# Optimization experiments

Measured on AMD Instinct MI355X. Metric: run time of the kernel, lower is better.

Reference implementation:

```python
import jax, jax.numpy as jnp
import numpy as np

T_MAX = 20
NUM_HEADS = 8
COMPLEXITY_W = 0.3
LN_EPS = 1e-5


def _layernorm(h, g, b):
    mu = jnp.mean(h, axis=-1, keepdims=True)
    var = jnp.var(h, axis=-1, keepdims=True)
    return (h - mu) / jnp.sqrt(var + LN_EPS) * g + b


def _gate_mlp(x, W1, b1, g, be, W2, b2, W3, b3):
    # Linear -> LayerNorm -> ReLU -> (Dropout=id in eval) -> Linear -> ReLU -> Linear -> Sigmoid
    h = jax.nn.relu(_layernorm(x @ W1 + b1, g, be))
    h = jax.nn.relu(h @ W2 + b2)
    return jax.nn.sigmoid(h @ W3 + b3)


def _adaptive_windows(x, p):
    S = x.shape[1]
    gate = _gate_mlp(x, p['gW1'], p['gb1'], p['gg'], p['gbe'], p['gW2'], p['gb2'], p['gW3'], p['gb3'])
    comp = _gate_mlp(x, p['cW1'], p['cb1'], p['cg'], p['cbe'], p['cW2'], p['cb2'], p['cW3'], p['cb3'])
    pos = jnp.linspace(0.8, 1.2, S, dtype=x.dtype).reshape(1, -1, 1)
    score = ((1.0 - COMPLEXITY_W) * gate + COMPLEXITY_W * comp) * pos
    T_i = jnp.clip(jnp.ceil(score[..., 0] * T_MAX), 1, T_MAX).astype(jnp.int32)  # [B,S]
    return T_i


def _spike_sum(x, T_i, alpha, beta):
    # LIF recurrence over T_MAX steps; accumulate masked spikes. x: [B,S,E]
    z = jnp.zeros_like(x)

    def step(carry, t):
        v, i, acc = carry
        active = (t < T_i).astype(x.dtype)[..., None]  # [B,S,1]
        i = alpha * i + x * active
        v = beta * v + i
        s = (v >= 1.0).astype(x.dtype)
        v = v * (1.0 - s)  # v_reset = 0
        return (v, i, acc + s * active), None

    (_, _, acc), _ = jax.lax.scan(step, (z, z, z), jnp.arange(T_MAX))
    return acc


def _forward(x, params):
    B, S, E = x.shape
    H, D = NUM_HEADS, E // NUM_HEADS
    q = x @ params['Wq']
    k = x @ params['Wk']
    v = x @ params['Wv']
    T_i = _adaptive_windows(x, params)
    q_sum = _spike_sum(q, T_i, params['alpha_q'], params['beta_q'])
    k_sum = _spike_sum(k, T_i, params['alpha_k'], params['beta_k'])
    v_mean = _spike_sum(v, T_i, params['alpha_v'], params['beta_v']) / T_MAX
    q_sum = q_sum.reshape(B, S, H, D)
    k_sum = k_sum.reshape(B, S, H, D)
    v_mean = v_mean.reshape(B, S, H, D)
    scale = D ** -0.5
    scores = jnp.einsum('bihd,bjhd->bhij', q_sum, k_sum) * scale
    w = jax.nn.softmax(scores, axis=-1)
    out = jnp.einsum('bhij,bjhd->bihd', w, v_mean).reshape(B, S, E)
    return out @ params['Wo'] + params['bo']


def setup_inputs() -> dict:
    key = jax.random.key(0)
    ks = iter(jax.random.split(key, 32))
    B, S, E = 4, 1024, 512
    f32 = jnp.float32

    def w(shape, scale=0.02):
        return jax.random.normal(next(ks), shape, dtype=f32) * scale

    inp = {
        'x': jax.random.normal(next(ks), (B, S, E), dtype=f32),
        'Wq': w((E, E)), 'Wk': w((E, E)), 'Wv': w((E, E)),
        'Wo': w((E, E)), 'bo': jnp.zeros((E,), f32),
        'gW1': w((E, 128)), 'gb1': jnp.zeros((128,), f32),
        'gg': jnp.ones((128,), f32), 'gbe': jnp.zeros((128,), f32),
        'gW2': w((128, 64)), 'gb2': jnp.zeros((64,), f32),
        'gW3': w((64, 1)), 'gb3': jnp.zeros((1,), f32),
        'cW1': w((E, 64)), 'cb1': jnp.zeros((64,), f32),
        'cg': jnp.ones((64,), f32), 'cbe': jnp.zeros((64,), f32),
        'cW2': w((64, 32)), 'cb2': jnp.zeros((32,), f32),
        'cW3': w((32, 1)), 'cb3': jnp.zeros((1,), f32),
        'alpha_q': jnp.asarray(np.exp(-1 / 5.0), f32), 'beta_q': jnp.asarray(np.exp(-1 / 20.0), f32),
        'alpha_k': jnp.asarray(np.exp(-1 / 5.0), f32), 'beta_k': jnp.asarray(np.exp(-1 / 20.0), f32),
        'alpha_v': jnp.asarray(np.exp(-1 / 5.0), f32), 'beta_v': jnp.asarray(np.exp(-1 / 20.0), f32),
    }
    return inp


def reference(x, Wq, Wk, Wv, Wo, bo,
              gW1, gb1, gg, gbe, gW2, gb2, gW3, gb3,
              cW1, cb1, cg, cbe, cW2, cb2, cW3, cb3,
              alpha_q, beta_q, alpha_k, beta_k, alpha_v, beta_v):
    params = dict(Wq=Wq, Wk=Wk, Wv=Wv, Wo=Wo, bo=bo,
                  gW1=gW1, gb1=gb1, gg=gg, gbe=gbe, gW2=gW2, gb2=gb2, gW3=gW3, gb3=gb3,
                  cW1=cW1, cb1=cb1, cg=cg, cbe=cbe, cW2=cW2, cb2=cb2, cW3=cW3, cb3=cb3,
                  alpha_q=alpha_q, beta_q=beta_q, alpha_k=alpha_k, beta_k=beta_k,
                  alpha_v=alpha_v, beta_v=beta_v)
    return _forward(x, params)
```

## Files before the change

### kernel.cpp

```cpp
#include <hip/hip_runtime.h>
#include <math.h>

#define SEQ   1024
#define EMB   512
#define NROWS 4096
#define LDP   72
#define GROWS 4

typedef __attribute__((ext_vector_type(8))) short short8;
typedef __attribute__((ext_vector_type(4))) float float4v;

__device__ __forceinline__ float bf2f(unsigned short s) {
    union { float f; unsigned u; } x; x.u = ((unsigned)s) << 16; return x.f;
}
__device__ __forceinline__ unsigned short f2bf(float f) {
    union { float f; unsigned u; } x; x.f = f;
    unsigned r = x.u + 0x7fffu + ((x.u >> 16) & 1u);
    return (unsigned short)(r >> 16);
}

__device__ __forceinline__ void gld16(const unsigned short* g, short* l) {
    __builtin_amdgcn_global_load_lds(
        (__attribute__((address_space(1))) void*)(g),
        (__attribute__((address_space(3))) void*)(l), 16, 0, 0);
}

__device__ __forceinline__ void split3(float x, unsigned short& h, unsigned short& m, unsigned short& l) {
    union { float f; unsigned u; } a; a.f = x;
    const unsigned rh = a.u + 0x7fffu + ((a.u >> 16) & 1u);
    h = (unsigned short)(rh >> 16);
    union { float f; unsigned u; } hf; hf.u = rh & 0xffff0000u;
    const float r1 = x - hf.f;
    a.f = r1;
    const unsigned rm = a.u + 0x7fffu + ((a.u >> 16) & 1u);
    m = (unsigned short)(rm >> 16);
    union { float f; unsigned u; } mf; mf.u = rm & 0xffff0000u;
    const float r2 = r1 - mf.f;
    l = f2bf(r2);
}

template<int H1, int H2>
__device__ __forceinline__ double mlp_eval(
    const double xs[GROWS][EMB], double* h1, double* h2, double* red,
    double* mu_s, double* var_s,
    const float* __restrict__ W1, const float* __restrict__ b1,
    const float* __restrict__ gam, const float* __restrict__ bet,
    const float* __restrict__ W2, const float* __restrict__ b2,
    const float* __restrict__ W3, const float* __restrict__ b3,
    int tid, int myrow)
{
    constexpr int S  = 256 / H1;
    constexpr int KS = EMB / S;

    {
        const int col = tid % H1, sk = tid / H1;
        double acc[GROWS] = {0.0, 0.0, 0.0, 0.0};
        const int kbeg = sk * KS;
        #pragma unroll 4
        for (int k = kbeg; k < kbeg + KS; ++k) {
            const double w = (double)W1[k * H1 + col];
            #pragma unroll
            for (int r = 0; r < GROWS; ++r) acc[r] += w * xs[r][k];
        }
        #pragma unroll
        for (int r = 0; r < GROWS; ++r) red[(sk * GROWS + r) * H1 + col] = acc[r];
    }
    __syncthreads();
    for (int idx = tid; idx < GROWS * H1; idx += 256) {
        const int r = idx / H1, cc = idx % H1;
        double s = 0.0;
        #pragma unroll
        for (int t = 0; t < S; ++t) s += red[(t * GROWS + r) * H1 + cc];
        h1[r * H1 + cc] = s + (double)b1[cc];
    }
    __syncthreads();

    {
        const int w = tid >> 6, l = tid & 63;
        double s = 0.0;
        for (int c = l; c < H1; c += 64) s += h1[w * H1 + c];
        #pragma unroll
        for (int off = 32; off >= 1; off >>= 1) s += __shfl_xor(s, off);
        if (l == 0) mu_s[w] = s / (double)H1;
    }
    __syncthreads();
    {
        const int w = tid >> 6, l = tid & 63;
        const double mu = mu_s[w];
        double s = 0.0;
        for (int c = l; c < H1; c += 64) { const double d = h1[w * H1 + c] - mu; s += d * d; }
        #pragma unroll
        for (int off = 32; off >= 1; off >>= 1) s += __shfl_xor(s, off);
        if (l == 0) var_s[w] = s / (double)H1;
    }
    __syncthreads();
    for (int idx = tid; idx < GROWS * H1; idx += 256) {
        const int r = idx / H1, cc = idx % H1;
        double hn = (h1[r * H1 + cc] - mu_s[r]) / sqrt(var_s[r] + 1e-5) * (double)gam[cc] + (double)bet[cc];
        h1[r * H1 + cc] = hn > 0.0 ? hn : 0.0;
    }
    __syncthreads();

    {
        const int col = tid % H2;
        const int r   = tid / H2;
        if (r < GROWS) {
            double acc = (double)b2[col];
            for (int k = 0; k < H1; ++k)
                acc += (double)W2[k * H2 + col] * h1[r * H1 + k];
            h2[r * H2 + col] = acc > 0.0 ? acc : 0.0;
        }
    }
    __syncthreads();

    {
        const int w = tid >> 6, l = tid & 63;
        double s = 0.0;
        for (int c = l; c < H2; c += 64) s += h2[w * H2 + c] * (double)W3[c];
        #pragma unroll
        for (int off = 32; off >= 1; off >>= 1) s += __shfl_xor(s, off);
        if (l == 0) mu_s[w] = s;
    }
    __syncthreads();
    double ret = 0.0;
    if (myrow >= 0) {
        const double z = mu_s[myrow] + (double)b3[0];
        ret = 1.0 / (1.0 + exp(-z));
    }
    return ret;
}

__global__ __launch_bounds__(256) void pre_kernel(
    const float* __restrict__ x,
    const float* __restrict__ gW1, const float* __restrict__ gb1,
    const float* __restrict__ gg,  const float* __restrict__ gbe,
    const float* __restrict__ gW2, const float* __restrict__ gb2,
    const float* __restrict__ gW3, const float* __restrict__ gb3,
    const float* __restrict__ cW1, const float* __restrict__ cb1,
    const float* __restrict__ cg,  const float* __restrict__ cbe,
    const float* __restrict__ cW2, const float* __restrict__ cb2,
    const float* __restrict__ cW3, const float* __restrict__ cb3,
    double* __restrict__ scores,
    const float* __restrict__ Wq, const float* __restrict__ Wk,
    const float* __restrict__ Wv, unsigned short* __restrict__ WL,
    unsigned short* __restrict__ XL,
    const float* __restrict__ Wo, unsigned short* __restrict__ WoT)
{
    __shared__ __align__(16) char smem[30784];
    const int bid = blockIdx.x;
    const int tid = threadIdx.x;

    if (bid < 2048) {
        double (*xs)[EMB] = (double(*)[EMB])smem;
        double* h1    = (double*)(smem + 16384);
        double* h2    = (double*)(smem + 20480);
        double* red   = (double*)(smem + 22528);
        double* mu_s  = (double*)(smem + 30720);
        double* var_s = (double*)(smem + 30752);

        const int gx = bid & 1023, gy = bid >> 10;
        const int row0 = gx * GROWS;

        for (int idx = tid; idx < GROWS * EMB; idx += 256) {
            const int r = idx >> 9, cc = idx & 511;
            xs[r][cc] = (double)x[(size_t)(row0 + r) * EMB + cc];
        }
        __syncthreads();

        const int myrow = (tid < GROWS) ? tid : -1;
        double v;
        if (gy == 0)
            v = mlp_eval<128, 64>(xs, h1, h2, red, mu_s, var_s,
                                  gW1, gb1, gg, gbe, gW2, gb2, gW3, gb3, tid, myrow);
        else
            v = mlp_eval<64, 32>(xs, h1, h2, red, mu_s, var_s,
                                 cW1, cb1, cg, cbe, cW2, cb2, cW3, cb3, tid, myrow);

        if (myrow >= 0)
            scores[(size_t)gy * NROWS + row0 + myrow] = v;

    } else if (bid < 3072) {
        unsigned short* Xh = XL;
        unsigned short* Xm = XL + (size_t)NROWS * EMB;
        unsigned short* Xl = Xm + (size_t)NROWS * EMB;
        const size_t i0 = ((size_t)(bid - 2048) * 256 + tid) * 8;
        const float4 a0 = *(const float4*)&x[i0];
        const float4 a1 = *(const float4*)&x[i0 + 4];
        const float av8[8] = {a0.x, a0.y, a0.z, a0.w, a1.x, a1.y, a1.z, a1.w};
        short8 ph, pm, pl;
        #pragma unroll
        for (int e = 0; e < 8; ++e) {
            unsigned short h, m, l;
            split3(av8[e], h, m, l);
            ph[e] = (short)h; pm[e] = (short)m; pl[e] = (short)l;
        }
        *(short8*)&Xh[i0] = ph;
        *(short8*)&Xm[i0] = pm;
        *(short8*)&Xl[i0] = pl;

    } else if (bid < 3264) {
        const int t = bid - 3072;
        const int z = t >> 6, rem = t & 63;
        const int k0 = (rem >> 3) * 64, n0 = (rem & 7) * 64;
        const float* __restrict__ W = (z == 0) ? Wq : (z == 1) ? Wk : Wv;
        unsigned short* Th = WL + (size_t)z * 3 * EMB * EMB;
        unsigned short* Tm = Th + (size_t)EMB * EMB;
        unsigned short* Tl = Tm + (size_t)EMB * EMB;

        float (*Ws)[68] = (float(*)[68])smem;
        #pragma unroll
        for (int it = 0; it < 4; ++it) {
            const int idx = it * 256 + tid;
            const int r = idx >> 4, c4 = (idx & 15) * 4;
            *(float4*)&Ws[r][c4] = *(const float4*)&W[(size_t)(k0 + r) * EMB + n0 + c4];
        }
        __syncthreads();
        #pragma unroll
        for (int it = 0; it < 2; ++it) {
            const int idx = it * 256 + tid;
            const int n = idx >> 3, k8 = (idx & 7) * 8;
            short8 ph, pm, pl;
            #pragma unroll
            for (int j = 0; j < 8; ++j) {
                unsigned short h, m, l;
                split3(Ws[k8 + j][n], h, m, l);
                ph[j] = (short)h; pm[j] = (short)m; pl[j] = (short)l;
            }
            const size_t o = (size_t)(n0 + n) * EMB + k0 + k8;
            *(short8*)&Th[o] = ph;
            *(short8*)&Tm[o] = pm;
            *(short8*)&Tl[o] = pl;
        }

    } else {
        const int t = bid - 3264;
        const int k0 = (t >> 3) * 64, n0 = (t & 7) * 64;
        unsigned short (*Ws)[72] = (unsigned short(*)[72])smem;
        #pragma unroll
        for (int it = 0; it < 4; ++it) {
            const int idx = it * 256 + tid;
            const int r = idx >> 4, c4 = (idx & 15) * 4;
            const float4 w4 = *(const float4*)&Wo[(size_t)(k0 + r) * EMB + n0 + c4];
            Ws[r][c4 + 0] = f2bf(w4.x); Ws[r][c4 + 1] = f2bf(w4.y);
            Ws[r][c4 + 2] = f2bf(w4.z); Ws[r][c4 + 3] = f2bf(w4.w);
        }
        __syncthreads();
        #pragma unroll
        for (int it = 0; it < 2; ++it) {
            const int idx = it * 256 + tid;
            const int n = idx >> 3, k8 = (idx & 7) * 8;
            short8 pack;
            #pragma unroll
            for (int j = 0; j < 8; ++j) pack[j] = (short)Ws[k8 + j][n];
            *(short8*)&WoT[(size_t)(n0 + n) * EMB + k0 + k8] = pack;
        }
    }
}

__global__ __launch_bounds__(256) void qkv_mfma_lif_kernel(
    const unsigned short* __restrict__ XL, const unsigned short* __restrict__ WL,
    const float* __restrict__ aq, const float* __restrict__ bq,
    const float* __restrict__ akp, const float* __restrict__ bkp,
    const float* __restrict__ av, const float* __restrict__ bv,
    const double* __restrict__ scores,
    unsigned short* __restrict__ q_sum, unsigned short* __restrict__ k_sum,
    unsigned short* __restrict__ v_mean)
{
    const int z = blockIdx.z;
    const unsigned short* __restrict__ WTh = WL + (size_t)z * 3 * EMB * EMB;
    const unsigned short* __restrict__ WTm = WTh + (size_t)EMB * EMB;
    const unsigned short* __restrict__ WTl = WTm + (size_t)EMB * EMB;
    const unsigned short* __restrict__ Xh = XL;
    const unsigned short* __restrict__ Xm = XL + (size_t)NROWS * EMB;
    const unsigned short* __restrict__ Xl = Xm + (size_t)NROWS * EMB;
    unsigned short* __restrict__ out = (z == 0) ? q_sum : (z == 1) ? k_sum : v_mean;
    const double alpha = (double)((z == 0) ? aq : (z == 1) ? akp : av)[0];
    const double beta  = (double)((z == 0) ? bq : (z == 1) ? bkp : bv)[0];

    const int phys = blockIdx.x + 8 * blockIdx.y;
    const int logical = (phys & 7) * 32 + (phys >> 3);
    const int bx = logical & 7, by = logical >> 3;
    const int row0 = by * 128, col0 = bx * 64;

    __shared__ __align__(16) short As0[3][4096], As1[3][4096];
    __shared__ __align__(16) short Bs0[3][2048], Bs1[3][2048];

    const int tid  = threadIdx.x;
    const int lane = tid & 63, wave = tid >> 6;
    const int qd = lane >> 4, c = lane & 15;
    const int wrow = wave * 32;

    const int kc8 = ((lane & 3) ^ ((lane >> 3) & 3)) * 8;
    const size_t ga0 = (size_t)(row0 + wave * 16 + (lane >> 2)) * EMB + kc8;
    const size_t ga1 = ga0 + (size_t)64 * EMB;
    const size_t gb  = (size_t)(col0 + wave * 16 + (lane >> 2)) * EMB + kc8;

    int arf[2], brf[4];
    #pragma unroll
    for (int i = 0; i < 2; ++i) {
        const int Ra = wrow + i * 16 + c;
        arf[i] = Ra * 32 + ((qd ^ ((Ra >> 1) & 3)) * 8);
    }
    #pragma unroll
    for (int j = 0; j < 4; ++j) {
        const int Rb = j * 16 + c;
        brf[j] = Rb * 32 + ((qd ^ ((Rb >> 1) & 3)) * 8);
    }

    float4v acc[2][4];
    #pragma unroll
    for (int i = 0; i < 2; ++i)
        #pragma unroll
        for (int j = 0; j < 4; ++j)
            acc[i][j] = (float4v){0.f, 0.f, 0.f, 0.f};

    auto STAGE = [&](short (*A_)[4096], short (*B_)[2048], int k0) {
        gld16(Xh  + ga0 + k0, &A_[0][wave * 512]);
        gld16(Xh  + ga1 + k0, &A_[0][2048 + wave * 512]);
        gld16(Xm  + ga0 + k0, &A_[1][wave * 512]);
        gld16(Xm  + ga1 + k0, &A_[1][2048 + wave * 512]);
        gld16(Xl  + ga0 + k0, &A_[2][wave * 512]);
        gld16(Xl  + ga1 + k0, &A_[2][2048 + wave * 512]);
        gld16(WTh + gb  + k0, &B_[0][wave * 512]);
        gld16(WTm + gb  + k0, &B_[1][wave * 512]);
        gld16(WTl + gb  + k0, &B_[2][wave * 512]);
    };
    auto COMPUTE = [&](const short (*A_)[4096], const short (*B_)[2048]) {
        short8 Afh[2], Afm[2], Afl[2];
        #pragma unroll
        for (int i = 0; i < 2; ++i) {
            Afh[i] = *(const short8*)&A_[0][arf[i]];
            Afm[i] = *(const short8*)&A_[1][arf[i]];
            Afl[i] = *(const short8*)&A_[2][arf[i]];
        }
        short8 Bfh[4], Bfm[4], Bfl[4];
        #pragma unroll
        for (int j = 0; j < 4; ++j) {
            Bfh[j] = *(const short8*)&B_[0][brf[j]];
            Bfm[j] = *(const short8*)&B_[1][brf[j]];
            Bfl[j] = *(const short8*)&B_[2][brf[j]];
        }
        #pragma unroll
        for (int i = 0; i < 2; ++i)
            #pragma unroll
            for (int j = 0; j < 4; ++j) {
                float4v t = acc[i][j];
                t = __builtin_amdgcn_mfma_f32_16x16x32_bf16(Afh[i], Bfh[j], t, 0, 0, 0);
                t = __builtin_amdgcn_mfma_f32_16x16x32_bf16(Afh[i], Bfm[j], t, 0, 0, 0);
                t = __builtin_amdgcn_mfma_f32_16x16x32_bf16(Afm[i], Bfh[j], t, 0, 0, 0);
                t = __builtin_amdgcn_mfma_f32_16x16x32_bf16(Afm[i], Bfm[j], t, 0, 0, 0);
                t = __builtin_amdgcn_mfma_f32_16x16x32_bf16(Afh[i], Bfl[j], t, 0, 0, 0);
                t = __builtin_amdgcn_mfma_f32_16x16x32_bf16(Afl[i], Bfh[j], t, 0, 0, 0);
                acc[i][j] = t;
            }
    };

    STAGE(As0, Bs0, 0);
    __syncthreads();
    for (int k0 = 0; k0 < EMB; k0 += 64) {
        STAGE(As1, Bs1, k0 + 32);
        COMPUTE(As0, Bs0);
        __syncthreads();
        if (k0 + 64 < EMB) STAGE(As0, Bs0, k0 + 64);
        COMPUTE(As1, Bs1);
        __syncthreads();
    }

    #pragma unroll
    for (int i = 0; i < 2; ++i)
        #pragma unroll
        for (int r = 0; r < 4; ++r) {
            const int gm = row0 + wrow + i * 16 + qd * 4 + r;
            const double g0 = scores[gm];
            const double c0 = scores[NROWS + gm];
            const int s = gm & (SEQ - 1);
            const double step = (1.2 - 0.8) / (double)(SEQ - 1);
            const double pos  = (double)s * step + 0.8;
            const double score = ((1.0 - 0.3) * g0 + 0.3 * c0) * pos;
            double td = ceil(score * 20.0);
            td = td < 1.0 ? 1.0 : (td > 20.0 ? 20.0 : td);
            const int T = (int)td;
            double cur0 = 0.0, cur1 = 0.0, cur2 = 0.0, cur3 = 0.0;
            double vm0 = 0.0, vm1 = 0.0, vm2 = 0.0, vm3 = 0.0;
            double sp0 = 0.0, sp1 = 0.0, sp2 = 0.0, sp3 = 0.0;
            const double xv0 = (double)acc[i][0][r];
            const double xv1 = (double)acc[i][1][r];
            const double xv2 = (double)acc[i][2][r];
            const double xv3 = (double)acc[i][3][r];
            for (int t = 0; t < T; ++t) {
                cur0 = alpha * cur0 + xv0; vm0 = beta * vm0 + cur0;
                if (vm0 >= 1.0) { sp0 += 1.0; vm0 = 0.0; }
                cur1 = alpha * cur1 + xv1; vm1 = beta * vm1 + cur1;
                if (vm1 >= 1.0) { sp1 += 1.0; vm1 = 0.0; }
                cur2 = alpha * cur2 + xv2; vm2 = beta * vm2 + cur2;
                if (vm2 >= 1.0) { sp2 += 1.0; vm2 = 0.0; }
                cur3 = alpha * cur3 + xv3; vm3 = beta * vm3 + cur3;
                if (vm3 >= 1.0) { sp3 += 1.0; vm3 = 0.0; }
            }
            if (z == 2) { sp0 /= 20.0; sp1 /= 20.0; sp2 /= 20.0; sp3 /= 20.0; }
            const size_t ob = (size_t)gm * EMB + col0 + c;
            out[ob +  0] = f2bf((float)sp0);
            out[ob + 16] = f2bf((float)sp1);
            out[ob + 32] = f2bf((float)sp2);
            out[ob + 48] = f2bf((float)sp3);
        }
}

__global__ __launch_bounds__(256) void attn_mfma_kernel(
    const unsigned short* __restrict__ q, const unsigned short* __restrict__ k,
    const unsigned short* __restrict__ v, unsigned short* __restrict__ attn_bf)
{
    __shared__ __align__(16) short Ks[64 * LDP];
    __shared__ __align__(16) short Pt[64 * LDP];
    __shared__ __align__(16) short Vt[64 * LDP];

    const int b = blockIdx.z, h = blockIdx.y;
    const int i0 = blockIdx.x * 64;
    const int tid  = threadIdx.x;
    const int wave = tid >> 6, lane = tid & 63;
    const int quad = lane >> 4, c = lane & 15;

    const unsigned short* Qb = q + ((size_t)b * SEQ + i0) * EMB + h * 64;
    const unsigned short* Kb = k + (size_t)b * SEQ * EMB + h * 64;
    const unsigned short* Vb = v + (size_t)b * SEQ * EMB + h * 64;

    short8 qf[2];
    {
        const int qrow = wave * 16 + c;
        #pragma unroll
        for (int ks = 0; ks < 2; ++ks) {
            short8 raw = *(const short8*)(Qb + (size_t)qrow * EMB + ks * 32 + quad * 8);
            short8 sc8;
            #pragma unroll
            for (int j = 0; j < 8; ++j)
                sc8[j] = (short)f2bf(bf2f((unsigned short)raw[j]) * 0.125f);
            qf[ks] = sc8;
        }
    }

    float m_r[4], l_r[4];
    float4v o[4];
    #pragma unroll
    for (int r = 0; r < 4; ++r) { m_r[r] = -1e30f; l_r[r] = 0.f; }
    #pragma unroll
    for (int nb = 0; nb < 4; ++nb)
        #pragma unroll
        for (int r = 0; r < 4; ++r) o[nb][r] = 0.f;

    for (int jt = 0; jt < SEQ / 64; ++jt) {
        #pragma unroll
        for (int it = 0; it < 2; ++it) {
            const int idx = it * 256 + tid;
            const int row = idx >> 3, ch = idx & 7;
            short8 val = *(const short8*)(Kb + (size_t)(jt * 64 + row) * EMB + ch * 8);
            *(short8*)&Ks[row * LDP + ch * 8] = val;
        }
        __syncthreads();

        float sc[4][4];
        #pragma unroll
        for (int nb = 0; nb < 4; ++nb) {
            float4v acc = {0.f, 0.f, 0.f, 0.f};
            #pragma unroll
            for (int ks = 0; ks < 2; ++ks) {
                short8 bfrag = *(const short8*)&Ks[(nb * 16 + c) * LDP + ks * 32 + quad * 8];
                acc = __builtin_amdgcn_mfma_f32_16x16x32_bf16(qf[ks], bfrag, acc, 0, 0, 0);
            }
            #pragma unroll
            for (int r = 0; r < 4; ++r) sc[nb][r] = acc[r];
        }

        float mnew[4], alpha[4];
        #pragma unroll
        for (int r = 0; r < 4; ++r) {
            float mx = fmaxf(fmaxf(sc[0][r], sc[1][r]), fmaxf(sc[2][r], sc[3][r]));
            #pragma unroll
            for (int off = 8; off >= 1; off >>= 1) mx = fmaxf(mx, __shfl_xor(mx, off));
            mnew[r]  = fmaxf(m_r[r], mx);
            alpha[r] = __expf(m_r[r] - mnew[r]);
            m_r[r]   = mnew[r];
        }
        float psum[4] = {0.f, 0.f, 0.f, 0.f};
        #pragma unroll
        for (int nb = 0; nb < 4; ++nb)
            #pragma unroll
            for (int r = 0; r < 4; ++r) {
                float p = __expf(sc[nb][r] - mnew[r]);
                psum[r] += p;
                Pt[(wave * 16 + quad * 4 + r) * LDP + nb * 16 + c] = (short)f2bf(p);
            }
        #pragma unroll
        for (int r = 0; r < 4; ++r) {
            float s = psum[r];
            #pragma unroll
            for (int off = 8; off >= 1; off >>= 1) s += __shfl_xor(s, off);
            l_r[r] = l_r[r] * alpha[r] + s;
            #pragma unroll
            for (int nb = 0; nb < 4; ++nb) o[nb][r] *= alpha[r];
        }

        {
            const int m = tid & 7, rp = tid >> 3;
            const int r = rp * 2;
            short8 v0 = *(const short8*)(Vb + (size_t)(jt * 64 + r) * EMB + m * 8);
            short8 v1 = *(const short8*)(Vb + (size_t)(jt * 64 + r + 1) * EMB + m * 8);
            const int rch = r >> 3, rlow = r & 7;
            #pragma unroll
            for (int i = 0; i < 8; ++i) {
                const int d = m * 8 + i;
                const int col = ((rch ^ m) << 3) + rlow;
                *(int*)&Vt[d * LDP + col] =
                    (int)((unsigned)(unsigned short)v0[i] |
                          ((unsigned)(unsigned short)v1[i] << 16));
            }
        }
        __syncthreads();

        short8 pf[2];
        #pragma unroll
        for (int ks = 0; ks < 2; ++ks)
            pf[ks] = *(const short8*)&Pt[(wave * 16 + c) * LDP + ks * 32 + quad * 8];
        #pragma unroll
        for (int nb = 0; nb < 4; ++nb) {
            float4v acc = o[nb];
            #pragma unroll
            for (int ks = 0; ks < 2; ++ks) {
                const int d = nb * 16 + c;
                const int kch = ks * 4 + quad;
                const int col = ((kch ^ (d >> 3)) << 3);
                short8 vfrag = *(const short8*)&Vt[d * LDP + col];
                acc = __builtin_amdgcn_mfma_f32_16x16x32_bf16(pf[ks], vfrag, acc, 0, 0, 0);
            }
            o[nb] = acc;
        }
    }

    #pragma unroll
    for (int r = 0; r < 4; ++r) {
        const float inv = 1.0f / l_r[r];
        const int row = i0 + wave * 16 + quad * 4 + r;
        #pragma unroll
        for (int nb = 0; nb < 4; ++nb)
            attn_bf[((size_t)b * SEQ + row) * EMB + h * 64 + nb * 16 + c] =
                f2bf(o[nb][r] * inv);
    }
}

__global__ __launch_bounds__(256) void out_gemm_kernel(
    const unsigned short* __restrict__ A,
    const unsigned short* __restrict__ BT,
    const float* __restrict__ bias, float* __restrict__ out)
{
    const int tid  = threadIdx.x;
    const int lane = tid & 63, wave = tid >> 6;
    const int qd = lane >> 4, c = lane & 15;
    const int wm = (wave & 1) * 32, wn = (wave >> 1) * 32;
    const int row0 = blockIdx.y * 64, col0 = blockIdx.x * 64;

    float4v acc[2][2];
    #pragma unroll
    for (int i = 0; i < 2; ++i)
        #pragma unroll
        for (int j = 0; j < 2; ++j)
            acc[i][j] = (float4v){0.f, 0.f, 0.f, 0.f};

    for (int k0 = 0; k0 < EMB; k0 += 32) {
        short8 af[2], bf[2];
        #pragma unroll
        for (int i = 0; i < 2; ++i)
            af[i] = *(const short8*)&A[(size_t)(row0 + wm + i * 16 + c) * EMB + k0 + qd * 8];
        #pragma unroll
        for (int j = 0; j < 2; ++j)
            bf[j] = *(const short8*)&BT[(size_t)(col0 + wn + j * 16 + c) * EMB + k0 + qd * 8];
        #pragma unroll
        for (int i = 0; i < 2; ++i)
            #pragma unroll
            for (int j = 0; j < 2; ++j)
                acc[i][j] = __builtin_amdgcn_mfma_f32_16x16x32_bf16(af[i], bf[j], acc[i][j], 0, 0, 0);
    }

    #pragma unroll
    for (int i = 0; i < 2; ++i)
        #pragma unroll
        for (int r = 0; r < 4; ++r) {
            const int gm = row0 + wm + i * 16 + qd * 4 + r;
            #pragma unroll
            for (int j = 0; j < 2; ++j) {
                const int gn = col0 + wn + j * 16 + c;
                out[(size_t)gm * EMB + gn] = acc[i][j][r] + bias[gn];
            }
        }
}

extern "C" void kernel_launch(void* const* d_in, const int* in_sizes, int n_in,
                              void* d_out, int out_size, void* d_ws, size_t ws_size,
                              hipStream_t stream)
{
    const float* x   = (const float*)d_in[0];
    const float* Wq  = (const float*)d_in[1];
    const float* Wk  = (const float*)d_in[2];
    const float* Wv  = (const float*)d_in[3];
    const float* Wo  = (const float*)d_in[4];
    const float* bo  = (const float*)d_in[5];
    const float* gW1 = (const float*)d_in[6];
    const float* gb1 = (const float*)d_in[7];
    const float* gg  = (const float*)d_in[8];
    const float* gbe = (const float*)d_in[9];
    const float* gW2 = (const float*)d_in[10];
    const float* gb2 = (const float*)d_in[11];
    const float* gW3 = (const float*)d_in[12];
    const float* gb3 = (const float*)d_in[13];
    const float* cW1 = (const float*)d_in[14];
    const float* cb1 = (const float*)d_in[15];
    const float* cg  = (const float*)d_in[16];
    const float* cbe = (const float*)d_in[17];
    const float* cW2 = (const float*)d_in[18];
    const float* cb2 = (const float*)d_in[19];
    const float* cW3 = (const float*)d_in[20];
    const float* cb3 = (const float*)d_in[21];
    const float* aq  = (const float*)d_in[22];
    const float* bq  = (const float*)d_in[23];
    const float* ak  = (const float*)d_in[24];
    const float* bk  = (const float*)d_in[25];
    const float* av  = (const float*)d_in[26];
    const float* bv  = (const float*)d_in[27];

    unsigned short* q_sum   = (unsigned short*)((char*)d_ws + 16384);
    unsigned short* k_sum   = q_sum   + (size_t)NROWS * EMB;
    unsigned short* v_mean  = k_sum   + (size_t)NROWS * EMB;
    unsigned short* attn_bf = v_mean  + (size_t)NROWS * EMB;
    unsigned short* WoT     = attn_bf + (size_t)NROWS * EMB;
    unsigned short* WL      = WoT     + (size_t)EMB * EMB;
    unsigned short* XLp     = WL      + (size_t)9 * EMB * EMB;
    double* scores          = (double*)(XLp + (size_t)3 * NROWS * EMB);
    float* out = (float*)d_out;

    pre_kernel<<<dim3(3328), dim3(256), 0, stream>>>(
        x, gW1, gb1, gg, gbe, gW2, gb2, gW3, gb3,
        cW1, cb1, cg, cbe, cW2, cb2, cW3, cb3, scores,
        Wq, Wk, Wv, WL, XLp, Wo, WoT);

    qkv_mfma_lif_kernel<<<dim3(EMB / 64, NROWS / 128, 3), dim3(256), 0, stream>>>(
        XLp, WL, aq, bq, ak, bk, av, bv, scores, q_sum, k_sum, v_mean);

    attn_mfma_kernel<<<dim3(SEQ / 64, 8, 4), dim3(256), 0, stream>>>(
        q_sum, k_sum, v_mean, attn_bf);

    out_gemm_kernel<<<dim3(EMB / 64, NROWS / 64), dim3(256), 0, stream>>>(
        attn_bf, WoT, bo, out);
}
```

Measured before the change: 264.4 us.

## Emit transposed V from QKV kernel and read V fragments directly in attention

The QKV+LIF kernel now also writes v_mean in a per-head transposed [b,h,d,seq] layout, so the attention kernel can load V MFMA fragments straight from global memory. This removes the per-tile shared-memory transpose of V and one barrier per tile. K staging is double-buffered in shared memory. Separately, the QKV GEMM drops its double-buffered LDS staging for a single buffer with two barriers per k-step, which shrinks LDS use but exposes load latency. The transposed writes are 2-byte scattered stores with large strides, and the global V fragment reads depend on L2 hits.

```diff
diff --git a/kernel.cpp b/kernel.cpp
--- a/kernel.cpp
+++ b/kernel.cpp
@@ -264,7 +264,7 @@
     const float* __restrict__ av, const float* __restrict__ bv,
     const double* __restrict__ scores,
     unsigned short* __restrict__ q_sum, unsigned short* __restrict__ k_sum,
-    unsigned short* __restrict__ v_mean)
+    unsigned short* __restrict__ v_mean, unsigned short* __restrict__ vt)
 {
     const int z = blockIdx.z;
     const unsigned short* __restrict__ WTh = WL + (size_t)z * 3 * EMB * EMB;
@@ -282,8 +282,8 @@
     const int bx = logical & 7, by = logical >> 3;
     const int row0 = by * 128, col0 = bx * 64;
 
-    __shared__ __align__(16) short As0[3][4096], As1[3][4096];
-    __shared__ __align__(16) short Bs0[3][2048], Bs1[3][2048];
+    __shared__ __align__(16) short As[3][4096];
+    __shared__ __align__(16) short Bs[3][2048];
 
     const int tid  = threadIdx.x;
     const int lane = tid & 63, wave = tid >> 6;
@@ -314,32 +314,34 @@
         for (int j = 0; j < 4; ++j)
             acc[i][j] = (float4v){0.f, 0.f, 0.f, 0.f};
 
-    auto STAGE = [&](short (*A_)[4096], short (*B_)[2048], int k0) {
-        gld16(Xh  + ga0 + k0, &A_[0][wave * 512]);
-        gld16(Xh  + ga1 + k0, &A_[0][2048 + wave * 512]);
-        gld16(Xm  + ga0 + k0, &A_[1][wave * 512]);
-        gld16(Xm  + ga1 + k0, &A_[1][2048 + wave * 512]);
-        gld16(Xl  + ga0 + k0, &A_[2][wave * 512]);
-        gld16(Xl  + ga1 + k0, &A_[2][2048 + wave * 512]);
-        gld16(WTh + gb  + k0, &B_[0][wave * 512]);
-        gld16(WTm + gb  + k0, &B_[1][wave * 512]);
-        gld16(WTl + gb  + k0, &B_[2][wave * 512]);
-    };
-    auto COMPUTE = [&](const short (*A_)[4096], const short (*B_)[2048]) {
+    for (int k0 = 0; k0 < EMB; k0 += 32) {
+        __syncthreads();
+        gld16(Xh  + ga0 + k0, &As[0][wave * 512]);
+        gld16(Xh  + ga1 + k0, &As[0][2048 + wave * 512]);
+        gld16(Xm  + ga0 + k0, &As[1][wave * 512]);
+        gld16(Xm  + ga1 + k0, &As[1][2048 + wave * 512]);
+        gld16(Xl  + ga0 + k0, &As[2][wave * 512]);
+        gld16(Xl  + ga1 + k0, &As[2][2048 + wave * 512]);
+        gld16(WTh + gb  + k0, &Bs[0][wave * 512]);
+        gld16(WTm + gb  + k0, &Bs[1][wave * 512]);
+        gld16(WTl + gb  + k0, &Bs[2][wave * 512]);
+        __syncthreads();
+
         short8 Afh[2], Afm[2], Afl[2];
         #pragma unroll
         for (int i = 0; i < 2; ++i) {
-            Afh[i] = *(const short8*)&A_[0][arf[i]];
-            Afm[i] = *(const short8*)&A_[1][arf[i]];
-            Afl[i] = *(const short8*)&A_[2][arf[i]];
+            Afh[i] = *(const short8*)&As[0][arf[i]];
+            Afm[i] = *(const short8*)&As[1][arf[i]];
+            Afl[i] = *(const short8*)&As[2][arf[i]];
         }
         short8 Bfh[4], Bfm[4], Bfl[4];
         #pragma unroll
         for (int j = 0; j < 4; ++j) {
-            Bfh[j] = *(const short8*)&B_[0][brf[j]];
-            Bfm[j] = *(const short8*)&B_[1][brf[j]];
-            Bfl[j] = *(const short8*)&B_[2][brf[j]];
-        }
+            Bfh[j] = *(const short8*)&Bs[0][brf[j]];
+            Bfm[j] = *(const short8*)&Bs[1][brf[j]];
+            Bfl[j] = *(const short8*)&Bs[2][brf[j]];
+        }
+
         #pragma unroll
         for (int i = 0; i < 2; ++i)
             #pragma unroll
@@ -353,17 +355,6 @@
                 t = __builtin_amdgcn_mfma_f32_16x16x32_bf16(Afl[i], Bfh[j], t, 0, 0, 0);
                 acc[i][j] = t;
             }
-    };
-
-    STAGE(As0, Bs0, 0);
-    __syncthreads();
-    for (int k0 = 0; k0 < EMB; k0 += 64) {
-        STAGE(As1, Bs1, k0 + 32);
-        COMPUTE(As0, Bs0);
-        __syncthreads();
-        if (k0 + 64 < EMB) STAGE(As0, Bs0, k0 + 64);
-        COMPUTE(As1, Bs1);
-        __syncthreads();
     }
 
     #pragma unroll
@@ -398,21 +389,33 @@
                 if (vm3 >= 1.0) { sp3 += 1.0; vm3 = 0.0; }
             }
             if (z == 2) { sp0 /= 20.0; sp1 /= 20.0; sp2 /= 20.0; sp3 /= 20.0; }
+            const unsigned short o0 = f2bf((float)sp0);
+            const unsigned short o1 = f2bf((float)sp1);
+            const unsigned short o2 = f2bf((float)sp2);
+            const unsigned short o3 = f2bf((float)sp3);
             const size_t ob = (size_t)gm * EMB + col0 + c;
-            out[ob +  0] = f2bf((float)sp0);
-            out[ob + 16] = f2bf((float)sp1);
-            out[ob + 32] = f2bf((float)sp2);
-            out[ob + 48] = f2bf((float)sp3);
+            out[ob +  0] = o0;
+            out[ob + 16] = o1;
+            out[ob + 32] = o2;
+            out[ob + 48] = o3;
+            if (z == 2) {
+                const int b = gm >> 10;
+                const int h = col0 >> 6;
+                const size_t vb = ((size_t)(b * 8 + h) * 64 + c) * SEQ + (gm & (SEQ - 1));
+                vt[vb +  0 * 16 * SEQ] = o0;
+                vt[vb +  1 * 16 * SEQ] = o1;
+                vt[vb +  2 * 16 * SEQ] = o2;
+                vt[vb +  3 * 16 * SEQ] = o3;
+            }
         }
 }
 
 __global__ __launch_bounds__(256) void attn_mfma_kernel(
     const unsigned short* __restrict__ q, const unsigned short* __restrict__ k,
-    const unsigned short* __restrict__ v, unsigned short* __restrict__ attn_bf)
+    const unsigned short* __restrict__ vt, unsigned short* __restrict__ attn_bf)
 {
-    __shared__ __align__(16) short Ks[64 * LDP];
+    __shared__ __align__(16) short Ks2[2][64 * LDP];
     __shared__ __align__(16) short Pt[64 * LDP];
-    __shared__ __align__(16) short Vt[64 * LDP];
 
     const int b = blockIdx.z, h = blockIdx.y;
     const int i0 = blockIdx.x * 64;
@@ -422,7 +425,7 @@
 
     const unsigned short* Qb = q + ((size_t)b * SEQ + i0) * EMB + h * 64;
     const unsigned short* Kb = k + (size_t)b * SEQ * EMB + h * 64;
-    const unsigned short* Vb = v + (size_t)b * SEQ * EMB + h * 64;
+    const unsigned short* VTb = vt + (size_t)(b * 8 + h) * 64 * SEQ;
 
     short8 qf[2];
     {
@@ -448,6 +451,7 @@
         for (int r = 0; r < 4; ++r) o[nb][r] = 0.f;
 
     for (int jt = 0; jt < SEQ / 64; ++jt) {
+        short* Ks = &Ks2[jt & 1][0];
         #pragma unroll
         for (int it = 0; it < 2; ++it) {
             const int idx = it * 256 + tid;
@@ -499,23 +503,6 @@
             for (int nb = 0; nb < 4; ++nb) o[nb][r] *= alpha[r];
         }
 
-        {
-            const int m = tid & 7, rp = tid >> 3;
-            const int r = rp * 2;
-            short8 v0 = *(const short8*)(Vb + (size_t)(jt * 64 + r) * EMB + m * 8);
-            short8 v1 = *(const short8*)(Vb + (size_t)(jt * 64 + r + 1) * EMB + m * 8);
-            const int rch = r >> 3, rlow = r & 7;
-            #pragma unroll
-            for (int i = 0; i < 8; ++i) {
-                const int d = m * 8 + i;
-                const int col = ((rch ^ m) << 3) + rlow;
-                *(int*)&Vt[d * LDP + col] =
-                    (int)((unsigned)(unsigned short)v0[i] |
-                          ((unsigned)(unsigned short)v1[i] << 16));
-            }
-        }
-        __syncthreads();
-
         short8 pf[2];
         #pragma unroll
         for (int ks = 0; ks < 2; ++ks)
@@ -523,12 +510,10 @@
         #pragma unroll
         for (int nb = 0; nb < 4; ++nb) {
             float4v acc = o[nb];
+            const int d = nb * 16 + c;
             #pragma unroll
             for (int ks = 0; ks < 2; ++ks) {
-                const int d = nb * 16 + c;
-                const int kch = ks * 4 + quad;
-                const int col = ((kch ^ (d >> 3)) << 3);
-                short8 vfrag = *(const short8*)&Vt[d * LDP + col];
+                short8 vfrag = *(const short8*)&VTb[(size_t)d * SEQ + jt * 64 + ks * 32 + quad * 8];
                 acc = __builtin_amdgcn_mfma_f32_16x16x32_bf16(pf[ks], vfrag, acc, 0, 0, 0);
             }
             o[nb] = acc;
@@ -633,6 +618,7 @@
     unsigned short* WL      = WoT     + (size_t)EMB * EMB;
     unsigned short* XLp     = WL      + (size_t)9 * EMB * EMB;
     double* scores          = (double*)(XLp + (size_t)3 * NROWS * EMB);
+    unsigned short* VT      = (unsigned short*)(scores + 2 * NROWS);
     float* out = (float*)d_out;
 
     pre_kernel<<<dim3(3328), dim3(256), 0, stream>>>(
@@ -641,10 +627,10 @@
         Wq, Wk, Wv, WL, XLp, Wo, WoT);
 
     qkv_mfma_lif_kernel<<<dim3(EMB / 64, NROWS / 128, 3), dim3(256), 0, stream>>>(
-        XLp, WL, aq, bq, ak, bk, av, bv, scores, q_sum, k_sum, v_mean);
+        XLp, WL, aq, bq, ak, bk, av, bv, scores, q_sum, k_sum, v_mean, VT);
 
     attn_mfma_kernel<<<dim3(SEQ / 64, 8, 4), dim3(256), 0, stream>>>(
-        q_sum, k_sum, v_mean, attn_bf);
+        q_sum, k_sum, VT, attn_bf);
 
     out_gemm_kernel<<<dim3(EMB / 64, NROWS / 64), dim3(256), 0, stream>>>(
         attn_bf, WoT, bo, out);
```

Result: no change. 269.3 us (+1.8%).

## Single-buffer QKV spike GEMM and stage output GEMM through LDS

Applied to the files above, without the earlier changes.

The QKV/spike GEMM kernel drops its double-buffered LDS staging and uses a single buffer with a barrier before and after each 32-wide k-step. This halves its shared-memory footprint, which may let more blocks run per CU, but it removes the overlap of loads with MFMA work. The output GEMM now loads A and B tiles into swizzled LDS via global_load_lds, with a remapped block order, instead of reading fragments directly from global memory. Each wave computes a 16x64 strip from the shared tiles.

```diff
diff --git a/kernel.cpp b/kernel.cpp
--- a/kernel.cpp
+++ b/kernel.cpp
@@ -282,8 +282,8 @@
     const int bx = logical & 7, by = logical >> 3;
     const int row0 = by * 128, col0 = bx * 64;
 
-    __shared__ __align__(16) short As0[3][4096], As1[3][4096];
-    __shared__ __align__(16) short Bs0[3][2048], Bs1[3][2048];
+    __shared__ __align__(16) short As[3][4096];
+    __shared__ __align__(16) short Bs[3][2048];
 
     const int tid  = threadIdx.x;
     const int lane = tid & 63, wave = tid >> 6;
@@ -314,32 +314,34 @@
         for (int j = 0; j < 4; ++j)
             acc[i][j] = (float4v){0.f, 0.f, 0.f, 0.f};
 
-    auto STAGE = [&](short (*A_)[4096], short (*B_)[2048], int k0) {
-        gld16(Xh  + ga0 + k0, &A_[0][wave * 512]);
-        gld16(Xh  + ga1 + k0, &A_[0][2048 + wave * 512]);
-        gld16(Xm  + ga0 + k0, &A_[1][wave * 512]);
-        gld16(Xm  + ga1 + k0, &A_[1][2048 + wave * 512]);
-        gld16(Xl  + ga0 + k0, &A_[2][wave * 512]);
-        gld16(Xl  + ga1 + k0, &A_[2][2048 + wave * 512]);
-        gld16(WTh + gb  + k0, &B_[0][wave * 512]);
-        gld16(WTm + gb  + k0, &B_[1][wave * 512]);
-        gld16(WTl + gb  + k0, &B_[2][wave * 512]);
-    };
-    auto COMPUTE = [&](const short (*A_)[4096], const short (*B_)[2048]) {
+    for (int k0 = 0; k0 < EMB; k0 += 32) {
+        __syncthreads();
+        gld16(Xh  + ga0 + k0, &As[0][wave * 512]);
+        gld16(Xh  + ga1 + k0, &As[0][2048 + wave * 512]);
+        gld16(Xm  + ga0 + k0, &As[1][wave * 512]);
+        gld16(Xm  + ga1 + k0, &As[1][2048 + wave * 512]);
+        gld16(Xl  + ga0 + k0, &As[2][wave * 512]);
+        gld16(Xl  + ga1 + k0, &As[2][2048 + wave * 512]);
+        gld16(WTh + gb  + k0, &Bs[0][wave * 512]);
+        gld16(WTm + gb  + k0, &Bs[1][wave * 512]);
+        gld16(WTl + gb  + k0, &Bs[2][wave * 512]);
+        __syncthreads();
+
         short8 Afh[2], Afm[2], Afl[2];
         #pragma unroll
         for (int i = 0; i < 2; ++i) {
-            Afh[i] = *(const short8*)&A_[0][arf[i]];
-            Afm[i] = *(const short8*)&A_[1][arf[i]];
-            Afl[i] = *(const short8*)&A_[2][arf[i]];
+            Afh[i] = *(const short8*)&As[0][arf[i]];
+            Afm[i] = *(const short8*)&As[1][arf[i]];
+            Afl[i] = *(const short8*)&As[2][arf[i]];
         }
         short8 Bfh[4], Bfm[4], Bfl[4];
         #pragma unroll
         for (int j = 0; j < 4; ++j) {
-            Bfh[j] = *(const short8*)&B_[0][brf[j]];
-            Bfm[j] = *(const short8*)&B_[1][brf[j]];
-            Bfl[j] = *(const short8*)&B_[2][brf[j]];
-        }
+            Bfh[j] = *(const short8*)&Bs[0][brf[j]];
+            Bfm[j] = *(const short8*)&Bs[1][brf[j]];
+            Bfl[j] = *(const short8*)&Bs[2][brf[j]];
+        }
+
         #pragma unroll
         for (int i = 0; i < 2; ++i)
             #pragma unroll
@@ -353,17 +355,6 @@
                 t = __builtin_amdgcn_mfma_f32_16x16x32_bf16(Afl[i], Bfh[j], t, 0, 0, 0);
                 acc[i][j] = t;
             }
-    };
-
-    STAGE(As0, Bs0, 0);
-    __syncthreads();
-    for (int k0 = 0; k0 < EMB; k0 += 64) {
-        STAGE(As1, Bs1, k0 + 32);
-        COMPUTE(As0, Bs0);
-        __syncthreads();
-        if (k0 + 64 < EMB) STAGE(As0, Bs0, k0 + 64);
-        COMPUTE(As1, Bs1);
-        __syncthreads();
     }
 
     #pragma unroll
@@ -551,44 +542,57 @@
     const unsigned short* __restrict__ BT,
     const float* __restrict__ bias, float* __restrict__ out)
 {
+    __shared__ __align__(16) short Ao[2048], Bo[2048];
+
     const int tid  = threadIdx.x;
     const int lane = tid & 63, wave = tid >> 6;
     const int qd = lane >> 4, c = lane & 15;
-    const int wm = (wave & 1) * 32, wn = (wave >> 1) * 32;
-    const int row0 = blockIdx.y * 64, col0 = blockIdx.x * 64;
-
-    float4v acc[2][2];
-    #pragma unroll
-    for (int i = 0; i < 2; ++i)
-        #pragma unroll
-        for (int j = 0; j < 2; ++j)
-            acc[i][j] = (float4v){0.f, 0.f, 0.f, 0.f};
+
+    const int phys = blockIdx.x + 8 * blockIdx.y;
+    const int logical = (phys & 7) * 64 + (phys >> 3);
+    const int bx = logical & 7, by = logical >> 3;
+    const int row0 = by * 64, col0 = bx * 64;
+
+    const int kc8 = ((lane & 3) ^ ((lane >> 3) & 3)) * 8;
+    const size_t ga = (size_t)(row0 + wave * 16 + (lane >> 2)) * EMB + kc8;
+    const size_t gb = (size_t)(col0 + wave * 16 + (lane >> 2)) * EMB + kc8;
+
+    int arf, brf[4];
+    {
+        const int Ra = wave * 16 + c;
+        arf = Ra * 32 + ((qd ^ ((Ra >> 1) & 3)) * 8);
+    }
+    #pragma unroll
+    for (int j = 0; j < 4; ++j) {
+        const int Rb = j * 16 + c;
+        brf[j] = Rb * 32 + ((qd ^ ((Rb >> 1) & 3)) * 8);
+    }
+
+    float4v acc[4];
+    #pragma unroll
+    for (int j = 0; j < 4; ++j) acc[j] = (float4v){0.f, 0.f, 0.f, 0.f};
 
     for (int k0 = 0; k0 < EMB; k0 += 32) {
-        short8 af[2], bf[2];
-        #pragma unroll
-        for (int i = 0; i < 2; ++i)
-            af[i] = *(const short8*)&A[(size_t)(row0 + wm + i * 16 + c) * EMB + k0 + qd * 8];
-        #pragma unroll
-        for (int j = 0; j < 2; ++j)
-            bf[j] = *(const short8*)&BT[(size_t)(col0 + wn + j * 16 + c) * EMB + k0 + qd * 8];
-        #pragma unroll
-        for (int i = 0; i < 2; ++i)
-            #pragma unroll
-            for (int j = 0; j < 2; ++j)
-                acc[i][j] = __builtin_amdgcn_mfma_f32_16x16x32_bf16(af[i], bf[j], acc[i][j], 0, 0, 0);
-    }
-
-    #pragma unroll
-    for (int i = 0; i < 2; ++i)
+        __syncthreads();
+        gld16(A  + ga + k0, &Ao[wave * 512]);
+        gld16(BT + gb + k0, &Bo[wave * 512]);
+        __syncthreads();
+
+        const short8 af = *(const short8*)&Ao[arf];
+        #pragma unroll
+        for (int j = 0; j < 4; ++j) {
+            const short8 bf = *(const short8*)&Bo[brf[j]];
+            acc[j] = __builtin_amdgcn_mfma_f32_16x16x32_bf16(af, bf, acc[j], 0, 0, 0);
+        }
+    }
+
+    #pragma unroll
+    for (int j = 0; j < 4; ++j)
         #pragma unroll
         for (int r = 0; r < 4; ++r) {
-            const int gm = row0 + wm + i * 16 + qd * 4 + r;
-            #pragma unroll
-            for (int j = 0; j < 2; ++j) {
-                const int gn = col0 + wn + j * 16 + c;
-                out[(size_t)gm * EMB + gn] = acc[i][j][r] + bias[gn];
-            }
+            const int gm = row0 + wave * 16 + qd * 4 + r;
+            const int gn = col0 + j * 16 + c;
+            out[(size_t)gm * EMB + gn] = acc[j][r] + bias[gn];
         }
 }
 
```

Measured after the change: 250.9 us. -5.1%, faster.
